# Kernel optimization log

Measured on AMD Instinct MI355X. Metric: run time of the kernel, lower is better.

## Reference

```python
import jax, jax.numpy as jnp
import numpy as np

A = 512   # input channels
B = 32    # number of capsule types
H4 = 16   # h*h pose dims per capsule


def setup_inputs() -> dict:
    key = jax.random.key(0)
    k1, k2, k3, k4, k5 = jax.random.split(key, 5)
    # Input feature map [N, A, H, W]
    x = jax.random.normal(k1, (64, A, 32, 32), dtype=jnp.float32)
    # Fused weights: B parallel 1x1 convs concatenated along out-channel dim.
    # Pose convs: B x Conv2d(A -> 16, k=1) -> [B*16, A]; activation convs: B x Conv2d(A -> 1) -> [B, A]
    bound = 1.0 / np.sqrt(A)  # PyTorch Conv2d default init range
    W_pose = jax.random.uniform(k2, (B * H4, A), minval=-bound, maxval=bound, dtype=jnp.float32)
    b_pose = jax.random.uniform(k3, (B * H4,), minval=-bound, maxval=bound, dtype=jnp.float32)
    W_act = jax.random.uniform(k4, (B, A), minval=-bound, maxval=bound, dtype=jnp.float32)
    b_act = jax.random.uniform(k5, (B,), minval=-bound, maxval=bound, dtype=jnp.float32)
    return {"x": x, "W_pose": W_pose, "b_pose": b_pose, "W_act": W_act, "b_act": b_act}


def reference(x, W_pose, b_pose, W_act, b_act):
    # 1x1 conv == channel contraction; fuse all 2*B tiny convs into two GEMMs.
    # poses: [N, B*16, H, W]
    poses = jnp.einsum('nahw,oa->nohw', x, W_pose) + b_pose[None, :, None, None]
    # activations: sigmoid([N, B, H, W])
    activations = jax.nn.sigmoid(jnp.einsum('nahw,oa->nohw', x, W_act) + b_act[None, :, None, None])
    return poses, activations
```

## Files before the change

### kernel.cpp

```cpp
#include <hip/hip_runtime.h>
#include <hip/hip_bf16.h>


typedef __attribute__((ext_vector_type(8))) short short8;
typedef __attribute__((ext_vector_type(4))) float f32x4;

#define A_CH   512
#define HW     1024
#define N_B    64
#define O_POSE 512
#define O_ACT  32
#define O_TOT  544
#define TO     128
#define TM     256
#define BK     32
#define NIT    (A_CH / BK)

__device__ __forceinline__ unsigned pk(float lo, float hi) {
    __hip_bfloat162 h = __float22bfloat162_rn(make_float2(lo, hi));
    return *reinterpret_cast<unsigned*>(&h);
}

__global__ __launch_bounds__(512, 4) void caps_fused_gemm(
    const float* __restrict__ x,
    const float* __restrict__ Wp,
    const float* __restrict__ bp,
    const float* __restrict__ Wa,
    const float* __restrict__ ba,
    float* __restrict__ out)
{
    __shared__ __align__(16) short ldsA[2][TO * BK];
    __shared__ __align__(16) short ldsB[2][TM * BK];

    const int tid = threadIdx.x;
    const int n   = blockIdx.z;
    const int o0  = blockIdx.y * TO;
    const int m0  = blockIdx.x * TM;

    const float* xn = x + (size_t)n * A_CH * HW + m0;

    const int ao = tid >> 2;
    const int ak = (tid & 3) * 8;
    const float* arow = nullptr;
    {
        int R = o0 + ao;
        if (R < O_POSE)     arow = Wp + (size_t)R * A_CH + ak;
        else if (R < O_TOT) arow = Wa + (size_t)(R - O_POSE) * A_CH + ak;
    }
    const int bm = tid & 255;
    const int bk = (tid >> 8) * 16;
    const float* bbase = xn + (size_t)bk * HW + bm;

    float4 a0, a1;
    float  breg[16];

    auto load_tiles = [&](int k0) {
        if (arow) {
            a0 = *(const float4*)(arow + k0);
            a1 = *(const float4*)(arow + k0 + 4);
        } else {
            a0 = make_float4(0.f, 0.f, 0.f, 0.f);
            a1 = a0;
        }
#pragma unroll
        for (int j = 0; j < 16; ++j)
            breg[j] = bbase[(size_t)(k0 + j) * HW];
    };

    const int aswz = 8 * ((ao >> 1) & 3);
    const int bswz = 8 * ((bm >> 1) & 3);

    auto store_tiles = [&](int buf) {
        short8 av;
        ((unsigned*)&av)[0] = pk(a0.x, a0.y);
        ((unsigned*)&av)[1] = pk(a0.z, a0.w);
        ((unsigned*)&av)[2] = pk(a1.x, a1.y);
        ((unsigned*)&av)[3] = pk(a1.z, a1.w);
        *(short8*)&ldsA[buf][ao * BK + (ak ^ aswz)] = av;

        short8 b0, b1;
#pragma unroll
        for (int j = 0; j < 4; ++j) {
            ((unsigned*)&b0)[j] = pk(breg[2 * j], breg[2 * j + 1]);
            ((unsigned*)&b1)[j] = pk(breg[8 + 2 * j], breg[9 + 2 * j]);
        }
        *(short8*)&ldsB[buf][bm * BK + (bk ^ bswz)]       = b0;
        *(short8*)&ldsB[buf][bm * BK + ((bk + 8) ^ bswz)] = b1;
    };

    const int lane = tid & 63;
    const int w    = tid >> 6;
    const int wo   = (w >> 2) * 64;
    const int wm   = (w & 3) * 64;
    const int l16  = lane & 15;
    const int g    = lane >> 4;

    f32x4 acc[4][4] = {};

    load_tiles(0);
    store_tiles(0);
    __syncthreads();

    for (int it = 0; it < NIT; ++it) {
        const int cur = it & 1;
        short8 aF[4], bF[4];
#pragma unroll
        for (int f = 0; f < 4; ++f) {
            int r = wo + f * 16 + l16;
            aF[f] = *(const short8*)&ldsA[cur][r * BK + ((g * 8) ^ (8 * ((r >> 1) & 3)))];
            int c = wm + f * 16 + l16;
            bF[f] = *(const short8*)&ldsB[cur][c * BK + ((g * 8) ^ (8 * ((c >> 1) & 3)))];
        }
        if (it + 1 < NIT) load_tiles((it + 1) * BK);
#pragma unroll
        for (int fo = 0; fo < 4; ++fo)
#pragma unroll
            for (int fm = 0; fm < 4; ++fm)
                acc[fo][fm] = __builtin_amdgcn_mfma_f32_16x16x32_bf16(
                    aF[fo], bF[fm], acc[fo][fm], 0, 0, 0);
        if (it + 1 < NIT) store_tiles(cur ^ 1);
        __syncthreads();
    }

    float* actOut = out + (size_t)N_B * O_POSE * HW;
    const size_t poseN = (size_t)n * O_POSE * HW;
    const size_t actN  = (size_t)n * O_ACT * HW;
#pragma unroll
    for (int fo = 0; fo < 4; ++fo) {
#pragma unroll
        for (int i = 0; i < 4; ++i) {
            int R = o0 + wo + fo * 16 + g * 4 + i;
            if (R >= O_TOT) continue;
            if (R < O_POSE) {
                float bias = bp[R];
#pragma unroll
                for (int fm = 0; fm < 4; ++fm) {
                    int cc = m0 + wm + fm * 16 + l16;
                    __builtin_nontemporal_store(acc[fo][fm][i] + bias,
                                                &out[poseN + (size_t)R * HW + cc]);
                }
            } else {
                float bias = ba[R - O_POSE];
#pragma unroll
                for (int fm = 0; fm < 4; ++fm) {
                    int cc = m0 + wm + fm * 16 + l16;
                    float v = acc[fo][fm][i] + bias;
                    __builtin_nontemporal_store(1.0f / (1.0f + __expf(-v)),
                                                &actOut[actN + (size_t)(R - O_POSE) * HW + cc]);
                }
            }
        }
    }
}

extern "C" void kernel_launch(void* const* d_in, const int* in_sizes, int n_in,
                              void* d_out, int out_size, void* d_ws, size_t ws_size,
                              hipStream_t stream) {
    (void)in_sizes; (void)n_in; (void)d_ws; (void)ws_size; (void)out_size;
    const float* x  = (const float*)d_in[0];
    const float* Wp = (const float*)d_in[1];
    const float* bp = (const float*)d_in[2];
    const float* Wa = (const float*)d_in[3];
    const float* ba = (const float*)d_in[4];
    dim3 grid(HW / TM, (O_TOT + TO - 1) / TO, N_B);
    caps_fused_gemm<<<grid, dim3(512), 0, stream>>>(x, Wp, bp, Wa, ba, (float*)d_out);
}
```

Baseline: 291.3 us.

## Deepen global-load prefetch to two stages with custom barrier and full unroll

Global loads of the weight and input tiles are now issued two K-iterations ahead into a double set of registers, so their latency is hidden behind more than one MFMA iteration. A raw s_barrier that waits only on LDS counters (not on vmcnt) replaces __syncthreads, so outstanding global loads stay in flight across the barrier. LDS offsets are precomputed and the K loop is fully unrolled. In exchange the register footprint roughly doubles for staging, and launch bounds drop from 4 to 2 blocks per CU, which lowers occupancy.

```diff
diff --git a/kernel.cpp b/kernel.cpp
--- a/kernel.cpp
+++ b/kernel.cpp
@@ -21,7 +21,11 @@
     return *reinterpret_cast<unsigned*>(&h);
 }
 
-__global__ __launch_bounds__(512, 4) void caps_fused_gemm(
+__device__ __forceinline__ void barrier_keep_loads() {
+    asm volatile("s_waitcnt lgkmcnt(0)\n\ts_barrier" ::: "memory");
+}
+
+__global__ __launch_bounds__(512, 2) void caps_fused_gemm(
     const float* __restrict__ x,
     const float* __restrict__ Wp,
     const float* __restrict__ bp,
@@ -51,41 +55,44 @@
     const int bk = (tid >> 8) * 16;
     const float* bbase = xn + (size_t)bk * HW + bm;
 
-    float4 a0, a1;
-    float  breg[16];
+    float4 a0r[2], a1r[2];
+    float  br[2][16];
 
-    auto load_tiles = [&](int k0) {
+    const int aswz = 8 * ((ao >> 1) & 3);
+    const int bswz = 8 * ((bm >> 1) & 3);
+    const int aoffW = ao * BK + (ak ^ aswz);
+    const int boffW0 = bm * BK + (bk ^ bswz);
+    const int boffW1 = bm * BK + ((bk + 8) ^ bswz);
+
+    auto load_tiles = [&](int rs, int k0) {
         if (arow) {
-            a0 = *(const float4*)(arow + k0);
-            a1 = *(const float4*)(arow + k0 + 4);
+            a0r[rs] = *(const float4*)(arow + k0);
+            a1r[rs] = *(const float4*)(arow + k0 + 4);
         } else {
-            a0 = make_float4(0.f, 0.f, 0.f, 0.f);
-            a1 = a0;
+            a0r[rs] = make_float4(0.f, 0.f, 0.f, 0.f);
+            a1r[rs] = a0r[rs];
         }
 #pragma unroll
         for (int j = 0; j < 16; ++j)
-            breg[j] = bbase[(size_t)(k0 + j) * HW];
+            br[rs][j] = bbase[(size_t)(k0 + j) * HW];
     };
 
-    const int aswz = 8 * ((ao >> 1) & 3);
-    const int bswz = 8 * ((bm >> 1) & 3);
-
-    auto store_tiles = [&](int buf) {
+    auto store_tiles = [&](int buf, int rs) {
         short8 av;
-        ((unsigned*)&av)[0] = pk(a0.x, a0.y);
-        ((unsigned*)&av)[1] = pk(a0.z, a0.w);
-        ((unsigned*)&av)[2] = pk(a1.x, a1.y);
-        ((unsigned*)&av)[3] = pk(a1.z, a1.w);
-        *(short8*)&ldsA[buf][ao * BK + (ak ^ aswz)] = av;
+        ((unsigned*)&av)[0] = pk(a0r[rs].x, a0r[rs].y);
+        ((unsigned*)&av)[1] = pk(a0r[rs].z, a0r[rs].w);
+        ((unsigned*)&av)[2] = pk(a1r[rs].x, a1r[rs].y);
+        ((unsigned*)&av)[3] = pk(a1r[rs].z, a1r[rs].w);
+        *(short8*)&ldsA[buf][aoffW] = av;
 
         short8 b0, b1;
 #pragma unroll
         for (int j = 0; j < 4; ++j) {
-            ((unsigned*)&b0)[j] = pk(breg[2 * j], breg[2 * j + 1]);
-            ((unsigned*)&b1)[j] = pk(breg[8 + 2 * j], breg[9 + 2 * j]);
+            ((unsigned*)&b0)[j] = pk(br[rs][2 * j],     br[rs][2 * j + 1]);
+            ((unsigned*)&b1)[j] = pk(br[rs][8 + 2 * j], br[rs][9 + 2 * j]);
         }
-        *(short8*)&ldsB[buf][bm * BK + (bk ^ bswz)]       = b0;
-        *(short8*)&ldsB[buf][bm * BK + ((bk + 8) ^ bswz)] = b1;
+        *(short8*)&ldsB[buf][boffW0] = b0;
+        *(short8*)&ldsB[buf][boffW1] = b1;
     };
 
     const int lane = tid & 63;
@@ -95,31 +102,43 @@
     const int l16  = lane & 15;
     const int g    = lane >> 4;
 
+    int aoffR[4], boffR[4];
+#pragma unroll
+    for (int f = 0; f < 4; ++f) {
+        int r = wo + f * 16 + l16;
+        aoffR[f] = r * BK + ((g * 8) ^ (8 * ((r >> 1) & 3)));
+        int c = wm + f * 16 + l16;
+        boffR[f] = c * BK + ((g * 8) ^ (8 * ((c >> 1) & 3)));
+    }
+
     f32x4 acc[4][4] = {};
 
-    load_tiles(0);
-    store_tiles(0);
-    __syncthreads();
+    load_tiles(0, 0);
+    load_tiles(1, BK);
+    store_tiles(0, 0);
+    barrier_keep_loads();
 
+#pragma unroll
     for (int it = 0; it < NIT; ++it) {
         const int cur = it & 1;
+        if (it + 2 < NIT) load_tiles(cur, (it + 2) * BK);
+
         short8 aF[4], bF[4];
 #pragma unroll
         for (int f = 0; f < 4; ++f) {
-            int r = wo + f * 16 + l16;
-            aF[f] = *(const short8*)&ldsA[cur][r * BK + ((g * 8) ^ (8 * ((r >> 1) & 3)))];
-            int c = wm + f * 16 + l16;
-            bF[f] = *(const short8*)&ldsB[cur][c * BK + ((g * 8) ^ (8 * ((c >> 1) & 3)))];
+            aF[f] = *(const short8*)&ldsA[cur][aoffR[f]];
+            bF[f] = *(const short8*)&ldsB[cur][boffR[f]];
         }
-        if (it + 1 < NIT) load_tiles((it + 1) * BK);
+        if (it + 1 < NIT) store_tiles(cur ^ 1, (it + 1) & 1);
+
 #pragma unroll
         for (int fo = 0; fo < 4; ++fo)
 #pragma unroll
             for (int fm = 0; fm < 4; ++fm)
                 acc[fo][fm] = __builtin_amdgcn_mfma_f32_16x16x32_bf16(
                     aF[fo], bF[fm], acc[fo][fm], 0, 0, 0);
-        if (it + 1 < NIT) store_tiles(cur ^ 1);
-        __syncthreads();
+
+        if (it + 1 < NIT) barrier_keep_loads();
     }
 
     float* actOut = out + (size_t)N_B * O_POSE * HW;
```

Measured after the change: 302.5 us. 3.8% more time.
